# Kernel optimization log

Measured on AMD Instinct MI355X. Metric: run time of the kernel, lower is better.

## Reference

```python
import jax, jax.numpy as jnp
import numpy as np

K = 5
PAD = (K - 1) // 2
EPS_NORM = 1e-8
MASS_BOUND = 1e-7


def _window_indices(H, W):
    # For each output location (y,x) and each offset (dy,dx) in the kxk window,
    # compute the flat index of (y+dy, x+dx) in prev space and a validity mask.
    ys, xs = jnp.meshgrid(jnp.arange(H), jnp.arange(W), indexing='ij')  # [H,W]
    offs = jnp.arange(-PAD, PAD + 1)
    dy, dx = jnp.meshgrid(offs, offs, indexing='ij')  # [k,k]
    py = ys[:, :, None, None] + dy[None, None]  # [H,W,k,k]
    px = xs[:, :, None, None] + dx[None, None]
    valid = (py >= 0) & (py < H) & (px >= 0) & (px < W)
    ploc = jnp.clip(py, 0, H - 1) * W + jnp.clip(px, 0, W - 1)
    HW, KK = H * W, K * K
    return ploc.reshape(HW, KK), valid.reshape(HW, KK)


def setup_inputs() -> dict:
    key = jax.random.key(0)
    k1, k2, k3 = jax.random.split(key, 3)
    N, D, H, W = 8, 64, 64, 64
    return {
        'cur_feat': jax.random.normal(k1, (N, D, H, W), dtype=jnp.float32),
        'prev_feat': jax.random.normal(k2, (N, D, H, W), dtype=jnp.float32),
        'prev_mem': jax.random.normal(k3, (N, D, H, W), dtype=jnp.float32),
    }


def reference(cur_feat, prev_feat, prev_mem):
    N, D, H, W = prev_mem.shape
    HW = H * W
    cur = cur_feat.reshape(N, -1, HW)   # [N,Dc,HW]
    prev = prev_feat.reshape(N, -1, HW)
    # torch.norm(x, 0) = number of nonzero entries (scalar per batch)
    nc = jnp.sum(cur != 0, axis=(1, 2)).astype(cur.dtype) + EPS_NORM   # [N]
    npv = jnp.sum(prev != 0, axis=(1, 2)).astype(prev.dtype) + EPS_NORM
    # full cost volume: [N, HW(cur loc), HW(prev loc)], negatives clamped to 0
    aff = jnp.einsum('ndp,ndq->npq', cur, prev) / (nc * npv)[:, None, None]
    aff = jnp.maximum(aff, 0.0)

    ploc, valid = _window_indices(H, W)        # [HW,KK]
    loc = jnp.arange(HW)[:, None]              # [HW,1]
    coef = aff[:, loc, ploc] * valid[None].astype(aff.dtype)  # [N,HW,KK]
    mass = jnp.sum(coef, axis=-1)              # [N,HW]
    zero_mass = jnp.abs(mass) < MASS_BOUND
    w = coef / jnp.where(zero_mass, 1.0, mass)[:, :, None]    # [N,HW,KK]

    pm = prev_mem.reshape(N, D, HW)            # [N,D,HW]
    pm_win = pm[:, :, ploc]                    # [N,D,HW,KK]
    val = jnp.einsum('npk,ndpk->ndp', w, pm_win)  # weighted aggregation
    out = jnp.where(zero_mass[:, None, :], pm, val)  # mass==0 -> passthrough
    return out.reshape(N, D, H, W)
```

## Files before the change

kernel.cpp:

```cpp
#include <hip/hip_runtime.h>

#define N_  8
#define D_  64
#define H_  64
#define W_  64
#define HW_ (H_ * W_)
#define KK  25

__global__ __launch_bounds__(256) void count_nz_kernel(
    const float4* __restrict__ cur, const float4* __restrict__ prev,
    const float4* __restrict__ pmv,
    unsigned int* __restrict__ pc, unsigned int* __restrict__ pq,
    unsigned int* __restrict__ pr)
{
    __shared__ unsigned int sc[4], sp[4], sr[4];
    const int t    = threadIdx.x;
    const int wid  = t >> 6;
    const int lane = t & 63;

    unsigned int wc = 0, wp = 0, wr = 0;
#pragma unroll
    for (int j = 0; j < 4; ++j) {
        int idx = blockIdx.x * 1024 + j * 256 + t;
        float4 a = cur[idx];
        float4 b = prev[idx];
        float4 m = pmv[idx];
        wc += (unsigned)__popcll(__ballot(a.x != 0.f));
        wc += (unsigned)__popcll(__ballot(a.y != 0.f));
        wc += (unsigned)__popcll(__ballot(a.z != 0.f));
        wc += (unsigned)__popcll(__ballot(a.w != 0.f));
        wp += (unsigned)__popcll(__ballot(b.x != 0.f));
        wp += (unsigned)__popcll(__ballot(b.y != 0.f));
        wp += (unsigned)__popcll(__ballot(b.z != 0.f));
        wp += (unsigned)__popcll(__ballot(b.w != 0.f));
        wr += (unsigned)__popcll(__ballot(m.x != 0.f));
        wr += (unsigned)__popcll(__ballot(m.y != 0.f));
        wr += (unsigned)__popcll(__ballot(m.z != 0.f));
        wr += (unsigned)__popcll(__ballot(m.w != 0.f));
    }
    if (lane == 0) { sc[wid] = wc; sp[wid] = wp; sr[wid] = wr; }
    __syncthreads();
    if (t == 0) {
        pc[blockIdx.x] = sc[0] + sc[1] + sc[2] + sc[3];
        pq[blockIdx.x] = sp[0] + sp[1] + sp[2] + sp[3];
        pr[blockIdx.x] = sr[0] + sr[1] + sr[2] + sr[3];
    }
}

__global__ __launch_bounds__(512, 4) void feature_align_kernel(
    const float* __restrict__ cur, const float* __restrict__ prev,
    const float* __restrict__ pm, float* __restrict__ out,
    const unsigned int* __restrict__ pc, const unsigned int* __restrict__ pq)
{
    __shared__ float red[4][KK][64];

    const int b    = blockIdx.x;
    const int n    = b >> 6;
    const int y    = b & 63;
    const int lane = threadIdx.x & 63;
    const int dg   = __builtin_amdgcn_readfirstlane(threadIdx.x >> 6);
    const int s    = lane >> 5;
    const int xq   = lane & 31;
    const int x0   = xq * 2;

    const unsigned laneoff = (unsigned)s * 4u * HW_ * 4u;
    int cb[3];
#pragma unroll
    for (int i = 0; i < 3; ++i)
        cb[i] = min(max(x0 - 2 + 2 * i, 0), W_ - 2);
    unsigned voff[5][3];
#pragma unroll
    for (int ky = 0; ky < 5; ++ky) {
        int qy = min(max(y + ky - 2, 0), H_ - 1);
#pragma unroll
        for (int i = 0; i < 3; ++i)
            voff[ky][i] = laneoff + (unsigned)((qy * W_ + cb[i]) * 4);
    }
    const unsigned curoff = laneoff + (unsigned)((y * W_ + x0) * 4);

    const size_t nbase = (size_t)n * D_ * HW_;
    const char* curb  = (const char*)(cur  + nbase + (size_t)dg * 8 * HW_);
    const char* prevb = (const char*)(prev + nbase + (size_t)dg * 8 * HW_);
    const char* pmb   = (const char*)(pm   + nbase + (size_t)dg * 8 * HW_);
    char*       outb  = (char*)(out + nbase + (size_t)dg * 8 * HW_);

    float2 pmc[4];
#pragma unroll
    for (int dd = 0; dd < 4; ++dd)
        pmc[dd] = *(const float2*)(pmb + (size_t)dd * HW_ * 4 + curoff);
    unsigned int ccnt = 0, vcnt = 0;
    if (dg == 0) {
        ccnt = pc[(n << 6) + lane];
        vcnt = pq[(n << 6) + lane];
    }

    float acc0[KK], acc1[KK];
#pragma unroll
    for (int k = 0; k < KK; ++k) { acc0[k] = 0.f; acc1[k] = 0.f; }

#pragma unroll
    for (int dd = 0; dd < 4; ++dd) {
        const char* cch = curb  + (size_t)dd * HW_ * 4;
        const char* pch = prevb + (size_t)dd * HW_ * 4;
        float2 c = *(const float2*)(cch + curoff);
        float2 t[5][3];
#pragma unroll
        for (int ky = 0; ky < 5; ++ky)
#pragma unroll
            for (int i = 0; i < 3; ++i)
                t[ky][i] = *(const float2*)(pch + voff[ky][i]);
#pragma unroll
        for (int ky = 0; ky < 5; ++ky) {
            float v[6] = { t[ky][0].x, t[ky][0].y, t[ky][1].x,
                           t[ky][1].y, t[ky][2].x, t[ky][2].y };
#pragma unroll
            for (int kx = 0; kx < 5; ++kx) {
                acc0[ky * 5 + kx] = fmaf(c.x, v[kx],     acc0[ky * 5 + kx]);
                acc1[ky * 5 + kx] = fmaf(c.y, v[kx + 1], acc1[ky * 5 + kx]);
            }
        }
    }

#pragma unroll
    for (int k = 0; k < KK; ++k) {
        acc0[k] += __shfl_xor(acc0[k], 32);
        acc1[k] += __shfl_xor(acc1[k], 32);
    }

    if (dg < 4) {
        if (s == 0)
#pragma unroll
            for (int k = 0; k < KK; ++k)
                *(float2*)&red[dg][k][x0] = make_float2(acc0[k], acc1[k]);
    }
    __syncthreads();
    if (dg >= 4) {
        if (s == 0)
#pragma unroll
            for (int k = 0; k < KK; ++k) {
                float2 t2 = *(float2*)&red[dg - 4][k][x0];
                t2.x += acc0[k]; t2.y += acc1[k];
                *(float2*)&red[dg - 4][k][x0] = t2;
            }
    }
    __syncthreads();

    if (dg == 0) {
        const int pix = lane;
        unsigned int cc = ccnt, vv = vcnt;
#pragma unroll
        for (int st = 32; st >= 1; st >>= 1) {
            cc += __shfl_xor(cc, st);
            vv += __shfl_xor(vv, st);
        }
        float scale = 1.0f / (((float)cc + 1e-8f) * ((float)vv + 1e-8f));

        float mass = 0.f;
        float cf[KK];
#pragma unroll
        for (int k = 0; k < KK; ++k) {
            float sm = red[0][k][pix] + red[1][k][pix]
                     + red[2][k][pix] + red[3][k][pix];
            int ky = k / 5, kx = k % 5;
            int py  = y + ky - 2;
            int pxc = pix + kx - 2;
            bool val = (py >= 0) && (py < H_) && (pxc >= 0) && (pxc < W_);
            float c = val ? fmaxf(sm * scale, 0.f) : 0.f;
            cf[k] = c;
            mass += c;
        }
        bool  zero = fabsf(mass) < 1e-7f;
        float inv  = zero ? 0.f : 1.0f / mass;
#pragma unroll
        for (int k = 0; k < KK; ++k) red[0][k][pix] = cf[k] * inv;
        red[1][0][pix] = zero ? 1.f : 0.f;
    }
    __syncthreads();

    const float zf0 = red[1][0][x0];
    const float zf1 = red[1][0][x0 + 1];

    if (zf0 != 0.f && zf1 != 0.f) {
#pragma unroll
        for (int dd = 0; dd < 4; ++dd)
            *(float2*)(outb + (size_t)dd * HW_ * 4 + curoff) = pmc[dd];
    } else {
        float w0[KK], w1[KK];
#pragma unroll
        for (int k = 0; k < KK; ++k) {
            float2 ww = *(float2*)&red[0][k][x0];
            w0[k] = ww.x; w1[k] = ww.y;
        }
#pragma unroll
        for (int dd = 0; dd < 4; ++dd) {
            const char* pch = pmb + (size_t)dd * HW_ * 4;
            float2 t2[5][3];
#pragma unroll
            for (int ky = 0; ky < 5; ++ky)
#pragma unroll
                for (int i = 0; i < 3; ++i)
                    t2[ky][i] = *(const float2*)(pch + voff[ky][i]);
            float v0 = 0.f, v1 = 0.f;
#pragma unroll
            for (int ky = 0; ky < 5; ++ky) {
                float v[6] = { t2[ky][0].x, t2[ky][0].y, t2[ky][1].x,
                               t2[ky][1].y, t2[ky][2].x, t2[ky][2].y };
#pragma unroll
                for (int kx = 0; kx < 5; ++kx) {
                    v0 = fmaf(w0[ky * 5 + kx], v[kx],     v0);
                    v1 = fmaf(w1[ky * 5 + kx], v[kx + 1], v1);
                }
            }
            float2 o;
            o.x = (zf0 != 0.f) ? pmc[dd].x : v0;
            o.y = (zf1 != 0.f) ? pmc[dd].y : v1;
            *(float2*)(outb + (size_t)dd * HW_ * 4 + curoff) = o;
        }
    }
}

extern "C" void kernel_launch(void* const* d_in, const int* in_sizes, int n_in,
                              void* d_out, int out_size, void* d_ws, size_t ws_size,
                              hipStream_t stream)
{
    const float* cur  = (const float*)d_in[0];
    const float* prev = (const float*)d_in[1];
    const float* pm   = (const float*)d_in[2];
    float*       out  = (float*)d_out;
    unsigned int* pc  = (unsigned int*)d_ws;
    unsigned int* pq  = pc + 512;
    unsigned int* pr  = pq + 512;

    count_nz_kernel<<<512, 256, 0, stream>>>(
        (const float4*)cur, (const float4*)prev, (const float4*)pm, pc, pq, pr);

    feature_align_kernel<<<512, 512, 0, stream>>>(cur, prev, pm, out, pc, pq);
}
```

Measured before the change: 94.00 us.

## Stage prev window rows in LDS and halve block size

```diff
diff --git a/kernel.cpp b/kernel.cpp
--- a/kernel.cpp
+++ b/kernel.cpp
@@ -47,123 +47,116 @@
     }
 }
 
-__global__ __launch_bounds__(512, 4) void feature_align_kernel(
+__global__ __launch_bounds__(256, 2) void feature_align_kernel(
     const float* __restrict__ cur, const float* __restrict__ prev,
     const float* __restrict__ pm, float* __restrict__ out,
     const unsigned int* __restrict__ pc, const unsigned int* __restrict__ pq)
 {
-    __shared__ float red[4][KK][64];
-
-    const int b    = blockIdx.x;
-    const int n    = b >> 6;
-    const int y    = b & 63;
-    const int lane = threadIdx.x & 63;
-    const int dg   = __builtin_amdgcn_readfirstlane(threadIdx.x >> 6);
-    const int s    = lane >> 5;
-    const int xq   = lane & 31;
-    const int x0   = xq * 2;
-
-    const unsigned laneoff = (unsigned)s * 4u * HW_ * 4u;
-    int cb[3];
-#pragma unroll
-    for (int i = 0; i < 3; ++i)
-        cb[i] = min(max(x0 - 2 + 2 * i, 0), W_ - 2);
-    unsigned voff[5][3];
-#pragma unroll
-    for (int ky = 0; ky < 5; ++ky) {
-        int qy = min(max(y + ky - 2, 0), H_ - 1);
-#pragma unroll
-        for (int i = 0; i < 3; ++i)
-            voff[ky][i] = laneoff + (unsigned)((qy * W_ + cb[i]) * 4);
-    }
-    const unsigned curoff = laneoff + (unsigned)((y * W_ + x0) * 4);
-
-    const size_t nbase = (size_t)n * D_ * HW_;
-    const char* curb  = (const char*)(cur  + nbase + (size_t)dg * 8 * HW_);
-    const char* prevb = (const char*)(prev + nbase + (size_t)dg * 8 * HW_);
-    const char* pmb   = (const char*)(pm   + nbase + (size_t)dg * 8 * HW_);
-    char*       outb  = (char*)(out + nbase + (size_t)dg * 8 * HW_);
-
-    float2 pmc[4];
-#pragma unroll
-    for (int dd = 0; dd < 4; ++dd)
-        pmc[dd] = *(const float2*)(pmb + (size_t)dd * HW_ * 4 + curoff);
+    __shared__ __align__(16) float ls[6400];
+
+    const int b   = blockIdx.x;
+    const int n   = b >> 6;
+    const int y   = b & 63;
+    const int tid = threadIdx.x;
+    const int xp  = tid & 31;
+    const int g   = tid >> 5;
+    const int x0  = xp * 2;
+
+    int qy[5];
+#pragma unroll
+    for (int ky = 0; ky < 5; ++ky)
+        qy[ky] = min(max(y + ky - 2, 0), H_ - 1);
+
+    const size_t chbase = (size_t)n * D_;
+
+    float2 cv[8], pmc[8];
+#pragma unroll
+    for (int j = 0; j < 8; ++j) {
+        int ch = ((j >> 1) << 4) + g * 2 + (j & 1);
+        const float* cp = cur + (chbase + ch) * HW_ + y * W_ + x0;
+        const float* mp = pm  + (chbase + ch) * HW_ + y * W_ + x0;
+        cv[j]  = *(const float2*)cp;
+        pmc[j] = *(const float2*)mp;
+    }
     unsigned int ccnt = 0, vcnt = 0;
-    if (dg == 0) {
-        ccnt = pc[(n << 6) + lane];
-        vcnt = pq[(n << 6) + lane];
+    if (tid < 64) {
+        ccnt = pc[(n << 6) + tid];
+        vcnt = pq[(n << 6) + tid];
     }
 
     float acc0[KK], acc1[KK];
 #pragma unroll
     for (int k = 0; k < KK; ++k) { acc0[k] = 0.f; acc1[k] = 0.f; }
 
-#pragma unroll
-    for (int dd = 0; dd < 4; ++dd) {
-        const char* cch = curb  + (size_t)dd * HW_ * 4;
-        const char* pch = prevb + (size_t)dd * HW_ * 4;
-        float2 c = *(const float2*)(cch + curoff);
-        float2 t[5][3];
-#pragma unroll
-        for (int ky = 0; ky < 5; ++ky)
-#pragma unroll
-            for (int i = 0; i < 3; ++i)
-                t[ky][i] = *(const float2*)(pch + voff[ky][i]);
-#pragma unroll
-        for (int ky = 0; ky < 5; ++ky) {
-            float v[6] = { t[ky][0].x, t[ky][0].y, t[ky][1].x,
-                           t[ky][1].y, t[ky][2].x, t[ky][2].y };
-#pragma unroll
-            for (int kx = 0; kx < 5; ++kx) {
-                acc0[ky * 5 + kx] = fmaf(c.x, v[kx],     acc0[ky * 5 + kx]);
-                acc1[ky * 5 + kx] = fmaf(c.y, v[kx + 1], acc1[ky * 5 + kx]);
+    const int sc_ = tid >> 4;
+    const int sxf = tid & 15;
+
+#pragma unroll
+    for (int cc = 0; cc < 4; ++cc) {
+#pragma unroll
+        for (int r = 0; r < 5; ++r) {
+            const float4 v4 = *(const float4*)(
+                prev + (chbase + cc * 16 + sc_) * HW_ + qy[r] * W_ + 4 * sxf);
+            *(float4*)&ls[sc_ * 360 + r * 72 + 4 + 4 * sxf] = v4;
+        }
+        __syncthreads();
+
+#pragma unroll
+        for (int j2 = 0; j2 < 2; ++j2) {
+            const int cloc = g * 2 + j2;
+            const float2 c2 = cv[cc * 2 + j2];
+#pragma unroll
+            for (int r = 0; r < 5; ++r) {
+                const float* row = &ls[cloc * 360 + r * 72];
+                float2 a = *(const float2*)&row[x0 + 2];
+                float2 bq = *(const float2*)&row[x0 + 4];
+                float2 d = *(const float2*)&row[x0 + 6];
+                float v[6] = { a.x, a.y, bq.x, bq.y, d.x, d.y };
+#pragma unroll
+                for (int kx = 0; kx < 5; ++kx) {
+                    acc0[r * 5 + kx] = fmaf(c2.x, v[kx],     acc0[r * 5 + kx]);
+                    acc1[r * 5 + kx] = fmaf(c2.y, v[kx + 1], acc1[r * 5 + kx]);
+                }
             }
         }
-    }
-
-#pragma unroll
-    for (int k = 0; k < KK; ++k) {
-        acc0[k] += __shfl_xor(acc0[k], 32);
-        acc1[k] += __shfl_xor(acc1[k], 32);
-    }
-
-    if (dg < 4) {
-        if (s == 0)
-#pragma unroll
-            for (int k = 0; k < KK; ++k)
-                *(float2*)&red[dg][k][x0] = make_float2(acc0[k], acc1[k]);
-    }
-    __syncthreads();
-    if (dg >= 4) {
-        if (s == 0)
-#pragma unroll
-            for (int k = 0; k < KK; ++k) {
-                float2 t2 = *(float2*)&red[dg - 4][k][x0];
-                t2.x += acc0[k]; t2.y += acc1[k];
-                *(float2*)&red[dg - 4][k][x0] = t2;
-            }
-    }
-    __syncthreads();
-
-    if (dg == 0) {
-        const int pix = lane;
-        unsigned int cc = ccnt, vv = vcnt;
+        __syncthreads();
+    }
+
+    if (g < 4) {
+#pragma unroll
+        for (int k = 0; k < KK; ++k)
+            *(float2*)&ls[g * 1600 + k * 64 + x0] = make_float2(acc0[k], acc1[k]);
+    }
+    __syncthreads();
+    if (g >= 4) {
+#pragma unroll
+        for (int k = 0; k < KK; ++k) {
+            float2 t2 = *(float2*)&ls[(g - 4) * 1600 + k * 64 + x0];
+            t2.x += acc0[k]; t2.y += acc1[k];
+            *(float2*)&ls[(g - 4) * 1600 + k * 64 + x0] = t2;
+        }
+    }
+    __syncthreads();
+
+    if (tid < 64) {
+        const int px = tid;
+        unsigned int cc2 = ccnt, vv = vcnt;
 #pragma unroll
         for (int st = 32; st >= 1; st >>= 1) {
-            cc += __shfl_xor(cc, st);
-            vv += __shfl_xor(vv, st);
-        }
-        float scale = 1.0f / (((float)cc + 1e-8f) * ((float)vv + 1e-8f));
+            cc2 += __shfl_xor(cc2, st);
+            vv  += __shfl_xor(vv, st);
+        }
+        float scale = 1.0f / (((float)cc2 + 1e-8f) * ((float)vv + 1e-8f));
 
         float mass = 0.f;
         float cf[KK];
 #pragma unroll
         for (int k = 0; k < KK; ++k) {
-            float sm = red[0][k][pix] + red[1][k][pix]
-                     + red[2][k][pix] + red[3][k][pix];
+            float sm = ls[k * 64 + px]        + ls[1600 + k * 64 + px]
+                     + ls[3200 + k * 64 + px] + ls[4800 + k * 64 + px];
             int ky = k / 5, kx = k % 5;
             int py  = y + ky - 2;
-            int pxc = pix + kx - 2;
+            int pxc = px + kx - 2;
             bool val = (py >= 0) && (py < H_) && (pxc >= 0) && (pxc < W_);
             float c = val ? fmaxf(sm * scale, 0.f) : 0.f;
             cf[k] = c;
@@ -172,39 +165,44 @@
         bool  zero = fabsf(mass) < 1e-7f;
         float inv  = zero ? 0.f : 1.0f / mass;
 #pragma unroll
-        for (int k = 0; k < KK; ++k) red[0][k][pix] = cf[k] * inv;
-        red[1][0][pix] = zero ? 1.f : 0.f;
-    }
-    __syncthreads();
-
-    const float zf0 = red[1][0][x0];
-    const float zf1 = red[1][0][x0 + 1];
+        for (int k = 0; k < KK; ++k) ls[k * 64 + px] = cf[k] * inv;
+        ls[1600 + px] = zero ? 1.f : 0.f;
+    }
+    __syncthreads();
+
+    const float zf0 = ls[1600 + x0];
+    const float zf1 = ls[1600 + x0 + 1];
 
     if (zf0 != 0.f && zf1 != 0.f) {
 #pragma unroll
-        for (int dd = 0; dd < 4; ++dd)
-            *(float2*)(outb + (size_t)dd * HW_ * 4 + curoff) = pmc[dd];
+        for (int j = 0; j < 8; ++j) {
+            int ch = ((j >> 1) << 4) + g * 2 + (j & 1);
+            *(float2*)(out + (chbase + ch) * HW_ + y * W_ + x0) = pmc[j];
+        }
     } else {
         float w0[KK], w1[KK];
 #pragma unroll
         for (int k = 0; k < KK; ++k) {
-            float2 ww = *(float2*)&red[0][k][x0];
-            w0[k] = ww.x; w1[k] = ww.y;
-        }
-#pragma unroll
-        for (int dd = 0; dd < 4; ++dd) {
-            const char* pch = pmb + (size_t)dd * HW_ * 4;
-            float2 t2[5][3];
-#pragma unroll
-            for (int ky = 0; ky < 5; ++ky)
+            w0[k] = ls[k * 64 + x0];
+            w1[k] = ls[k * 64 + x0 + 1];
+        }
+        int cb[3];
+#pragma unroll
+        for (int i = 0; i < 3; ++i)
+            cb[i] = min(max(x0 - 2 + 2 * i, 0), W_ - 2);
+#pragma unroll
+        for (int j = 0; j < 8; ++j) {
+            int ch = ((j >> 1) << 4) + g * 2 + (j & 1);
+            const float* pch = pm + (chbase + ch) * HW_;
+            float v0 = 0.f, v1 = 0.f;
+#pragma unroll
+            for (int ky = 0; ky < 5; ++ky) {
+                float2 t2[3];
 #pragma unroll
                 for (int i = 0; i < 3; ++i)
-                    t2[ky][i] = *(const float2*)(pch + voff[ky][i]);
-            float v0 = 0.f, v1 = 0.f;
-#pragma unroll
-            for (int ky = 0; ky < 5; ++ky) {
-                float v[6] = { t2[ky][0].x, t2[ky][0].y, t2[ky][1].x,
-                               t2[ky][1].y, t2[ky][2].x, t2[ky][2].y };
+                    t2[i] = *(const float2*)(pch + qy[ky] * W_ + cb[i]);
+                float v[6] = { t2[0].x, t2[0].y, t2[1].x,
+                               t2[1].y, t2[2].x, t2[2].y };
 #pragma unroll
                 for (int kx = 0; kx < 5; ++kx) {
                     v0 = fmaf(w0[ky * 5 + kx], v[kx],     v0);
@@ -212,9 +210,9 @@
                 }
             }
             float2 o;
-            o.x = (zf0 != 0.f) ? pmc[dd].x : v0;
-            o.y = (zf1 != 0.f) ? pmc[dd].y : v1;
-            *(float2*)(outb + (size_t)dd * HW_ * 4 + curoff) = o;
+            o.x = (zf0 != 0.f) ? pmc[j].x : v0;
+            o.y = (zf1 != 0.f) ? pmc[j].y : v1;
+            *(float2*)(out + (chbase + ch) * HW_ + y * W_ + x0) = o;
         }
     }
 }
@@ -234,5 +232,5 @@
     count_nz_kernel<<<512, 256, 0, stream>>>(
         (const float4*)cur, (const float4*)prev, (const float4*)pm, pc, pq, pr);
 
-    feature_align_kernel<<<512, 512, 0, stream>>>(cur, prev, pm, out, pc, pq);
+    feature_align_kernel<<<512, 256, 0, stream>>>(cur, prev, pm, out, pc, pq);
 }
```

New measurement: 90.71 us. 1.04x faster.

## Halve block size and give each thread eight channels instead of four

Applied to the files above, without the earlier changes.

```diff
diff --git a/kernel.cpp b/kernel.cpp
--- a/kernel.cpp
+++ b/kernel.cpp
@@ -47,23 +47,22 @@
     }
 }
 
-__global__ __launch_bounds__(512, 4) void feature_align_kernel(
+__global__ __launch_bounds__(256, 2) void feature_align_kernel(
     const float* __restrict__ cur, const float* __restrict__ prev,
     const float* __restrict__ pm, float* __restrict__ out,
     const unsigned int* __restrict__ pc, const unsigned int* __restrict__ pq)
 {
     __shared__ float red[4][KK][64];
 
-    const int b    = blockIdx.x;
-    const int n    = b >> 6;
-    const int y    = b & 63;
-    const int lane = threadIdx.x & 63;
-    const int dg   = __builtin_amdgcn_readfirstlane(threadIdx.x >> 6);
-    const int s    = lane >> 5;
-    const int xq   = lane & 31;
-    const int x0   = xq * 2;
-
-    const unsigned laneoff = (unsigned)s * 4u * HW_ * 4u;
+    const int b   = blockIdx.x;
+    const int n   = b & 7;
+    const int y   = b >> 3;
+    const int tid = threadIdx.x;
+    const int xp  = tid & 31;
+    const int g   = tid >> 5;
+    const int x0  = xp * 2;
+
+    const unsigned goff = (unsigned)g * 8u * HW_ * 4u;
     int cb[3];
 #pragma unroll
     for (int i = 0; i < 3; ++i)
@@ -74,24 +73,24 @@
         int qy = min(max(y + ky - 2, 0), H_ - 1);
 #pragma unroll
         for (int i = 0; i < 3; ++i)
-            voff[ky][i] = laneoff + (unsigned)((qy * W_ + cb[i]) * 4);
-    }
-    const unsigned curoff = laneoff + (unsigned)((y * W_ + x0) * 4);
+            voff[ky][i] = goff + (unsigned)((qy * W_ + cb[i]) * 4);
+    }
+    const unsigned curoff = goff + (unsigned)((y * W_ + x0) * 4);
 
     const size_t nbase = (size_t)n * D_ * HW_;
-    const char* curb  = (const char*)(cur  + nbase + (size_t)dg * 8 * HW_);
-    const char* prevb = (const char*)(prev + nbase + (size_t)dg * 8 * HW_);
-    const char* pmb   = (const char*)(pm   + nbase + (size_t)dg * 8 * HW_);
-    char*       outb  = (char*)(out + nbase + (size_t)dg * 8 * HW_);
-
-    float2 pmc[4];
-#pragma unroll
-    for (int dd = 0; dd < 4; ++dd)
+    const char* curb  = (const char*)(cur  + nbase);
+    const char* prevb = (const char*)(prev + nbase);
+    const char* pmb   = (const char*)(pm   + nbase);
+    char*       outb  = (char*)(out + nbase);
+
+    float2 pmc[8];
+#pragma unroll
+    for (int dd = 0; dd < 8; ++dd)
         pmc[dd] = *(const float2*)(pmb + (size_t)dd * HW_ * 4 + curoff);
     unsigned int ccnt = 0, vcnt = 0;
-    if (dg == 0) {
-        ccnt = pc[(n << 6) + lane];
-        vcnt = pq[(n << 6) + lane];
+    if (tid < 64) {
+        ccnt = pc[(n << 6) + tid];
+        vcnt = pq[(n << 6) + tid];
     }
 
     float acc0[KK], acc1[KK];
@@ -99,7 +98,7 @@
     for (int k = 0; k < KK; ++k) { acc0[k] = 0.f; acc1[k] = 0.f; }
 
 #pragma unroll
-    for (int dd = 0; dd < 4; ++dd) {
+    for (int dd = 0; dd < 8; ++dd) {
         const char* cch = curb  + (size_t)dd * HW_ * 4;
         const char* pch = prevb + (size_t)dd * HW_ * 4;
         float2 c = *(const float2*)(cch + curoff);
@@ -121,32 +120,24 @@
         }
     }
 
-#pragma unroll
-    for (int k = 0; k < KK; ++k) {
-        acc0[k] += __shfl_xor(acc0[k], 32);
-        acc1[k] += __shfl_xor(acc1[k], 32);
-    }
-
-    if (dg < 4) {
-        if (s == 0)
-#pragma unroll
-            for (int k = 0; k < KK; ++k)
-                *(float2*)&red[dg][k][x0] = make_float2(acc0[k], acc1[k]);
-    }
-    __syncthreads();
-    if (dg >= 4) {
-        if (s == 0)
-#pragma unroll
-            for (int k = 0; k < KK; ++k) {
-                float2 t2 = *(float2*)&red[dg - 4][k][x0];
-                t2.x += acc0[k]; t2.y += acc1[k];
-                *(float2*)&red[dg - 4][k][x0] = t2;
-            }
-    }
-    __syncthreads();
-
-    if (dg == 0) {
-        const int pix = lane;
+    if (g < 4) {
+#pragma unroll
+        for (int k = 0; k < KK; ++k)
+            *(float2*)&red[g][k][x0] = make_float2(acc0[k], acc1[k]);
+    }
+    __syncthreads();
+    if (g >= 4) {
+#pragma unroll
+        for (int k = 0; k < KK; ++k) {
+            float2 t2 = *(float2*)&red[g - 4][k][x0];
+            t2.x += acc0[k]; t2.y += acc1[k];
+            *(float2*)&red[g - 4][k][x0] = t2;
+        }
+    }
+    __syncthreads();
+
+    if (tid < 64) {
+        const int px = tid;
         unsigned int cc = ccnt, vv = vcnt;
 #pragma unroll
         for (int st = 32; st >= 1; st >>= 1) {
@@ -159,11 +150,11 @@
         float cf[KK];
 #pragma unroll
         for (int k = 0; k < KK; ++k) {
-            float sm = red[0][k][pix] + red[1][k][pix]
-                     + red[2][k][pix] + red[3][k][pix];
+            float sm = red[0][k][px] + red[1][k][px]
+                     + red[2][k][px] + red[3][k][px];
             int ky = k / 5, kx = k % 5;
             int py  = y + ky - 2;
-            int pxc = pix + kx - 2;
+            int pxc = px + kx - 2;
             bool val = (py >= 0) && (py < H_) && (pxc >= 0) && (pxc < W_);
             float c = val ? fmaxf(sm * scale, 0.f) : 0.f;
             cf[k] = c;
@@ -172,8 +163,8 @@
         bool  zero = fabsf(mass) < 1e-7f;
         float inv  = zero ? 0.f : 1.0f / mass;
 #pragma unroll
-        for (int k = 0; k < KK; ++k) red[0][k][pix] = cf[k] * inv;
-        red[1][0][pix] = zero ? 1.f : 0.f;
+        for (int k = 0; k < KK; ++k) red[0][k][px] = cf[k] * inv;
+        red[1][0][px] = zero ? 1.f : 0.f;
     }
     __syncthreads();
 
@@ -182,17 +173,17 @@
 
     if (zf0 != 0.f && zf1 != 0.f) {
 #pragma unroll
-        for (int dd = 0; dd < 4; ++dd)
+        for (int dd = 0; dd < 8; ++dd)
             *(float2*)(outb + (size_t)dd * HW_ * 4 + curoff) = pmc[dd];
     } else {
         float w0[KK], w1[KK];
 #pragma unroll
         for (int k = 0; k < KK; ++k) {
-            float2 ww = *(float2*)&red[0][k][x0];
-            w0[k] = ww.x; w1[k] = ww.y;
-        }
-#pragma unroll
-        for (int dd = 0; dd < 4; ++dd) {
+            w0[k] = red[0][k][x0];
+            w1[k] = red[0][k][x0 + 1];
+        }
+#pragma unroll
+        for (int dd = 0; dd < 8; ++dd) {
             const char* pch = pmb + (size_t)dd * HW_ * 4;
             float2 t2[5][3];
 #pragma unroll
@@ -234,5 +225,5 @@
     count_nz_kernel<<<512, 256, 0, stream>>>(
         (const float4*)cur, (const float4*)prev, (const float4*)pm, pc, pq, pr);
 
-    feature_align_kernel<<<512, 512, 0, stream>>>(cur, prev, pm, out, pc, pq);
+    feature_align_kernel<<<512, 256, 0, stream>>>(cur, prev, pm, out, pc, pq);
 }
```

New measurement: 91.15 us. 3.0% less time.
